# Performance work log

Hardware: AMD Instinct MI355X
Metric: run time of the kernel (lower is better)

The kernel has to match this reference:

```python
import jax, jax.numpy as jnp
import numpy as np

IN_CH, IN_DIM, OUT_CH, OUT_DIM = 16, 32, 32, 32
NUM_ITERS = 3
EPS = 1e-11


def setup_inputs() -> dict:
    key = jax.random.key(0)
    kx, kw = jax.random.split(key)
    B, N = 32, 128
    x = jax.random.normal(kx, (B, N, IN_CH, IN_DIM), dtype=jnp.float32)
    # learned transform, matches torch Parameter randn(1,1,in_ch,out_ch,in_dim,out_dim)
    W = jax.random.normal(kw, (IN_CH, OUT_CH, IN_DIM, OUT_DIM), dtype=jnp.float32)
    return {"x": x, "W": W, "number_of_nodes": N}


def squash(s):
    # s: [B, 1, out_ch, out_dim]; squash along capsule dim (axis=3)
    mag_sq = jnp.sum(s * s, axis=3, keepdims=True)
    mag = jnp.sqrt(mag_sq) + EPS
    a_j = mag_sq / (1.0 + mag_sq)
    return a_j * (s / mag), a_j


def reference(x, W, number_of_nodes):
    B, N = x.shape[0], x.shape[1]
    # u_hat[b,n,c,o,j] = sum_i x[b,n,c,i] * W[c,o,i,j]
    u_hat = jnp.einsum('bnci,coij->bncoj', x, W)
    u_hat = u_hat.reshape(B, N * IN_CH, OUT_CH, OUT_DIM)

    b_ij = jnp.zeros((B, N * IN_CH, OUT_CH, 1), dtype=u_hat.dtype)
    v_j = a_j = None
    for _ in range(NUM_ITERS):
        c_ij = jax.nn.softmax(b_ij, axis=1)          # softmax over input capsules
        s_j = jnp.sum(c_ij * u_hat, axis=1, keepdims=True)  # [B,1,out_ch,out_dim]
        v_j, a_j = squash(s_j)
        # agreement: broadcast v_j over input-capsule dim (no explicit cat)
        u_vj = jnp.sum(u_hat * v_j, axis=3, keepdims=True)
        b_ij = b_ij + u_vj
    return v_j, a_j
```

## Files before the change

kernel.cpp:

```cpp
#include <hip/hip_runtime.h>
#include <math.h>

#define BB 32
#define NN 128
#define CC 16
#define OO 32
#define II 32
#define JJ 32
#define MM (NN*CC)
#define WP (JJ+1)
static constexpr float EPS_ = 1e-11f;


__global__ __launch_bounds__(1024) void k_transpose(
    const float* __restrict__ x, float* __restrict__ xT) {
  int b = blockIdx.x >> 4, c = blockIdx.x & 15;
  __shared__ __align__(16) float xsT[II][NN + 4];
  int tid = threadIdx.x;
  {
    int n = tid >> 3, i4 = (tid & 7) * 4;
    float4 v = *(const float4*)(x + (((size_t)(b * NN + n)) * CC + c) * II + i4);
    xsT[i4 + 0][n] = v.x; xsT[i4 + 1][n] = v.y;
    xsT[i4 + 2][n] = v.z; xsT[i4 + 3][n] = v.w;
  }
  __syncthreads();
  {
    int i = tid >> 5, n4 = tid & 31;
    float4 v = *(const float4*)(&xsT[i][n4 * 4]);
    ((float4*)(xT + ((size_t)(b * CC + c)) * II * NN))[tid] = v;
  }
}

__device__ __forceinline__ float rs16(float p[16], int l) {
  bool u2 = (l >> 1) & 1, u4 = (l >> 2) & 1, u8 = (l >> 3) & 1, u16 = (l >> 4) & 1;
  #pragma unroll
  for (int k = 0; k < 8; ++k) {
    float s0 = u2 ? p[k] : p[k + 8];
    float r0 = __shfl_xor(s0, 2);
    p[k] = (u2 ? p[k + 8] : p[k]) + r0;
  }
  #pragma unroll
  for (int k = 0; k < 4; ++k) {
    float s0 = u4 ? p[k] : p[k + 4];
    float r0 = __shfl_xor(s0, 4);
    p[k] = (u4 ? p[k + 4] : p[k]) + r0;
  }
  #pragma unroll
  for (int k = 0; k < 2; ++k) {
    float s0 = u8 ? p[k] : p[k + 2];
    float r0 = __shfl_xor(s0, 8);
    p[k] = (u8 ? p[k + 2] : p[k]) + r0;
  }
  {
    float s0 = u16 ? p[0] : p[1];
    float r0 = __shfl_xor(s0, 16);
    p[0] = (u16 ? p[1] : p[0]) + r0;
  }
  p[0] += __shfl_xor(p[0], 32);
  return p[0];
}

__global__ __launch_bounds__(1024, 4) void k_route(
    const float* __restrict__ xT, const float* __restrict__ W,
    float* __restrict__ out) {
  int bid = blockIdx.x;
  int b = bid & 31, o0 = (bid >> 5) * 2;
  int tid = threadIdx.x;

  __shared__ float Ws[CC * 2 * II * WP];
  __shared__ __align__(16) float bijL[2][CC][NN];
  __shared__ float cw[2][CC][II];
  __shared__ float partA[2][CC][JJ];
  __shared__ float vs[2][JJ];
  __shared__ float redM[CC][2], redE[CC][2];
  __shared__ float smx[2], srin[2];

  {
    int q = tid & 7, r0 = tid >> 3;
    #pragma unroll
    for (int k = 0; k < 8; ++k) {
      int rowid = r0 + k * 128;
      int c = rowid >> 6, o = (rowid >> 5) & 1, i = rowid & 31;
      float4 v = *(const float4*)(W + ((((size_t)c * OO + o0 + o) * II + i) * JJ) + q * 4);
      float* dst = &Ws[rowid * WP + q * 4];
      dst[0] = v.x; dst[1] = v.y; dst[2] = v.z; dst[3] = v.w;
    }
  }

  int l = tid & 63;
  int c = tid >> 6, n4 = l >> 1, s = l & 1;
  const float4* xTb = (const float4*)(xT + (size_t)b * CC * II * NN);
  const float4* xp  = xTb + c * (II * NN / 4) + (s * 16) * (NN / 4) + n4;
  float4 xv[16];
  #pragma unroll
  for (int q = 0; q < 16; ++q) xv[q] = xp[q * (NN / 4)];

  {
    int o = tid >> 9, ci = (tid >> 5) & 15, m4i = tid & 31;
    *(float4*)(&bijL[o][ci][m4i * 4]) = make_float4(0.f, 0.f, 0.f, 0.f);
    if (tid < 2) { smx[tid] = 0.f; srin[tid] = 1.0f / (float)MM; }
  }
  __syncthreads();

  for (int it = 0; it < 3; ++it) {
    {
      int qf = ((l >> 1) & 1) * 8 + ((l >> 2) & 1) * 4
             + ((l >> 3) & 1) * 2 + ((l >> 4) & 1);
      #pragma unroll
      for (int o = 0; o < 2; ++o) {
        float4 bb = *(const float4*)(&bijL[o][c][n4 * 4]);
        float m = smx[o], ri = srin[o];
        float cfx = __expf(bb.x - m) * ri, cfy = __expf(bb.y - m) * ri;
        float cfz = __expf(bb.z - m) * ri, cfw = __expf(bb.w - m) * ri;
        float p[16];
        #pragma unroll
        for (int q = 0; q < 16; ++q)
          p[q] = xv[q].x*cfx + xv[q].y*cfy + xv[q].z*cfz + xv[q].w*cfw;
        float r = rs16(p, l);
        if ((l & 32) == 0) cw[o][c][s * 16 + qf] = r;
      }
    }
    __syncthreads();

    {
      int o = tid >> 9, cA = (tid >> 5) & 15, j = tid & 31;
      const float* wsp = &Ws[((cA * 2 + o) * II) * WP + j];
      float acc = 0.f;
      #pragma unroll 8
      for (int i = 0; i < II; ++i)
        acc += cw[o][cA][i] * wsp[i * WP];
      partA[o][cA][j] = acc;
    }
    __syncthreads();

    if (tid < 64) {
      int o = tid >> 5, j = tid & 31;
      float sA = 0.f;
      #pragma unroll
      for (int cR = 0; cR < CC; ++cR) sA += partA[o][cR][j];
      float msq = sA * sA;
      #pragma unroll
      for (int off = 16; off > 0; off >>= 1) msq += __shfl_xor(msq, off);
      float mag = sqrtf(msq) + EPS_;
      float a   = msq / (1.0f + msq);
      float vvq = a * sA / mag;
      if (it == 2) {
        int row = b * OO + (o0 + o);
        out[(size_t)row * JJ + j] = vvq;
        if (j == 0) out[BB * OO * JJ + row] = a;
      } else {
        vs[o][j] = vvq;
      }
    }
    if (it == 2) break;
    __syncthreads();

    {
      int o = tid >> 9, cW = (tid >> 5) & 15, i = tid & 31;
      const float* wsr = &Ws[((cW * 2 + o) * II + i) * WP];
      float acc = 0.f;
      #pragma unroll 8
      for (int j = 0; j < JJ; ++j)
        acc += wsr[j] * vs[o][j];
      cw[o][cW][i] = acc;
    }
    __syncthreads();

    {
      float4 ac0 = make_float4(0.f,0.f,0.f,0.f);
      float4 ac1 = make_float4(0.f,0.f,0.f,0.f);
      #pragma unroll
      for (int q = 0; q < 16; ++q) {
        int i = s * 16 + q;
        float w0 = cw[0][c][i], w1 = cw[1][c][i];
        ac0.x += xv[q].x * w0; ac0.y += xv[q].y * w0;
        ac0.z += xv[q].z * w0; ac0.w += xv[q].w * w0;
        ac1.x += xv[q].x * w1; ac1.y += xv[q].y * w1;
        ac1.z += xv[q].z * w1; ac1.w += xv[q].w * w1;
      }
      ac0.x += __shfl_xor(ac0.x, 1); ac0.y += __shfl_xor(ac0.y, 1);
      ac0.z += __shfl_xor(ac0.z, 1); ac0.w += __shfl_xor(ac0.w, 1);
      ac1.x += __shfl_xor(ac1.x, 1); ac1.y += __shfl_xor(ac1.y, 1);
      ac1.z += __shfl_xor(ac1.z, 1); ac1.w += __shfl_xor(ac1.w, 1);
      float4 r = (s == 0) ? ac0 : ac1;
      float4 bb = *(const float4*)(&bijL[s][c][n4 * 4]);
      r.x += bb.x; r.y += bb.y; r.z += bb.z; r.w += bb.w;
      *(float4*)(&bijL[s][c][n4 * 4]) = r;

      float m4 = fmaxf(fmaxf(r.x, r.y), fmaxf(r.z, r.w));
      #pragma unroll
      for (int off = 2; off <= 32; off <<= 1) m4 = fmaxf(m4, __shfl_xor(m4, off));
      int wave = tid >> 6;
      if ((tid & 63) <= 1) redM[wave][s] = m4;
      __syncthreads();
      float mo = redM[0][s];
      #pragma unroll
      for (int w2 = 1; w2 < CC; ++w2) mo = fmaxf(mo, redM[w2][s]);
      float ex = __expf(r.x - mo), ey = __expf(r.y - mo),
            ez = __expf(r.z - mo), ew = __expf(r.w - mo);
      float e = ex + ey + ez + ew;
      #pragma unroll
      for (int off = 2; off <= 32; off <<= 1) e += __shfl_xor(e, off);
      if ((tid & 63) <= 1) redE[wave][s] = e;
      __syncthreads();
      if (tid < 2) {
        float ss = 0.f, mm = redM[0][tid];
        #pragma unroll
        for (int w2 = 0; w2 < CC; ++w2) ss += redE[w2][tid];
        #pragma unroll
        for (int w2 = 1; w2 < CC; ++w2) mm = fmaxf(mm, redM[w2][tid]);
        smx[tid]  = mm;
        srin[tid] = 1.0f / ss;
      }
    }
    __syncthreads();
  }
}

extern "C" void kernel_launch(void* const* d_in, const int* in_sizes, int n_in,
                              void* d_out, int out_size, void* d_ws, size_t ws_size,
                              hipStream_t stream) {
  const float* x = (const float*)d_in[0];
  const float* W = (const float*)d_in[1];
  (void)in_sizes; (void)n_in;
  float* out = (float*)d_out; (void)out_size;

  float* xT = (float*)d_ws;
  (void)ws_size;

  k_transpose<<<BB * CC, 1024, 0, stream>>>(x, xT);
  k_route<<<BB * (OO / 2), 1024, 0, stream>>>(xT, W, out);
}
```

Baseline: 107.2 us.

## Cut block barriers via wave-local cw ownership and online softmax reduction

Remaps the cw consumer/producer thread indexing so each wave reads only cw values written by its own wave, which lets two __syncthreads be dropped. The softmax max and sum are now computed in one pass (online rescaling of per-wave sums), removing another barrier and the single-thread finalize. The max and reciprocal are kept in registers and swapped between lanes with a shuffle instead of going through shared memory. This relies on wave-level ordering of shared-memory writes and reads without an explicit barrier, and adds extra exp work per thread in the final reduction.

```diff
diff --git a/kernel.cpp b/kernel.cpp
--- a/kernel.cpp
+++ b/kernel.cpp
@@ -69,11 +69,10 @@
 
   __shared__ float Ws[CC * 2 * II * WP];
   __shared__ __align__(16) float bijL[2][CC][NN];
-  __shared__ float cw[2][CC][II];
+  __shared__ __align__(16) float cw[2][CC][II];
   __shared__ float partA[2][CC][JJ];
   __shared__ float vs[2][JJ];
   __shared__ float redM[CC][2], redE[CC][2];
-  __shared__ float smx[2], srin[2];
 
   {
     int q = tid & 7, r0 = tid >> 3;
@@ -98,8 +97,9 @@
   {
     int o = tid >> 9, ci = (tid >> 5) & 15, m4i = tid & 31;
     *(float4*)(&bijL[o][ci][m4i * 4]) = make_float4(0.f, 0.f, 0.f, 0.f);
-    if (tid < 2) { smx[tid] = 0.f; srin[tid] = 1.0f / (float)MM; }
-  }
+  }
+  float mo0 = 0.f, mo1 = 0.f;
+  float rin0 = 1.0f / (float)MM, rin1 = rin0;
   __syncthreads();
 
   for (int it = 0; it < 3; ++it) {
@@ -109,7 +109,8 @@
       #pragma unroll
       for (int o = 0; o < 2; ++o) {
         float4 bb = *(const float4*)(&bijL[o][c][n4 * 4]);
-        float m = smx[o], ri = srin[o];
+        float m  = (o == 0) ? mo0 : mo1;
+        float ri = (o == 0) ? rin0 : rin1;
         float cfx = __expf(bb.x - m) * ri, cfy = __expf(bb.y - m) * ri;
         float cfz = __expf(bb.z - m) * ri, cfw = __expf(bb.w - m) * ri;
         float p[16];
@@ -120,10 +121,9 @@
         if ((l & 32) == 0) cw[o][c][s * 16 + qf] = r;
       }
     }
-    __syncthreads();
-
-    {
-      int o = tid >> 9, cA = (tid >> 5) & 15, j = tid & 31;
+
+    {
+      int cA = tid >> 6, o = (tid >> 5) & 1, j = tid & 31;
       const float* wsp = &Ws[((cA * 2 + o) * II) * WP + j];
       float acc = 0.f;
       #pragma unroll 8
@@ -156,7 +156,7 @@
     __syncthreads();
 
     {
-      int o = tid >> 9, cW = (tid >> 5) & 15, i = tid & 31;
+      int cW = tid >> 6, o = (tid >> 5) & 1, i = tid & 31;
       const float* wsr = &Ws[((cW * 2 + o) * II + i) * WP];
       float acc = 0.f;
       #pragma unroll 8
@@ -164,7 +164,6 @@
         acc += wsr[j] * vs[o][j];
       cw[o][cW][i] = acc;
     }
-    __syncthreads();
 
     {
       float4 ac0 = make_float4(0.f,0.f,0.f,0.f);
@@ -190,30 +189,25 @@
       float m4 = fmaxf(fmaxf(r.x, r.y), fmaxf(r.z, r.w));
       #pragma unroll
       for (int off = 2; off <= 32; off <<= 1) m4 = fmaxf(m4, __shfl_xor(m4, off));
+      float e = __expf(r.x - m4) + __expf(r.y - m4)
+              + __expf(r.z - m4) + __expf(r.w - m4);
+      #pragma unroll
+      for (int off = 2; off <= 32; off <<= 1) e += __shfl_xor(e, off);
       int wave = tid >> 6;
-      if ((tid & 63) <= 1) redM[wave][s] = m4;
+      if ((tid & 63) <= 1) { redM[wave][s] = m4; redE[wave][s] = e; }
       __syncthreads();
       float mo = redM[0][s];
       #pragma unroll
       for (int w2 = 1; w2 < CC; ++w2) mo = fmaxf(mo, redM[w2][s]);
-      float ex = __expf(r.x - mo), ey = __expf(r.y - mo),
-            ez = __expf(r.z - mo), ew = __expf(r.w - mo);
-      float e = ex + ey + ez + ew;
-      #pragma unroll
-      for (int off = 2; off <= 32; off <<= 1) e += __shfl_xor(e, off);
-      if ((tid & 63) <= 1) redE[wave][s] = e;
-      __syncthreads();
-      if (tid < 2) {
-        float ss = 0.f, mm = redM[0][tid];
-        #pragma unroll
-        for (int w2 = 0; w2 < CC; ++w2) ss += redE[w2][tid];
-        #pragma unroll
-        for (int w2 = 1; w2 < CC; ++w2) mm = fmaxf(mm, redM[w2][tid]);
-        smx[tid]  = mm;
-        srin[tid] = 1.0f / ss;
-      }
-    }
-    __syncthreads();
+      float ss = 0.f;
+      #pragma unroll
+      for (int w2 = 0; w2 < CC; ++w2)
+        ss += redE[w2][s] * __expf(redM[w2][s] - mo);
+      float rin = 1.0f / ss;
+      float moO = __shfl_xor(mo, 1), rinO = __shfl_xor(rin, 1);
+      mo0  = (s == 0) ? mo  : moO;   mo1  = (s == 0) ? moO  : mo;
+      rin0 = (s == 0) ? rin : rinO;  rin1 = (s == 0) ? rinO : rin;
+    }
   }
 }
 
```

New measurement: 109.0 us. No clear change (+1.7%).
